# Kernel optimization log

Measured on AMD Instinct MI355X. Metric: run time of the kernel, lower is better.

Reference implementation:

```python
import jax, jax.numpy as jnp
import numpy as np

B, L, C = 16, 450, 768
MID = 256
K = 8912
TEMP = 0.07
ENT_TEMP = 0.01
EPS_NORM = 1e-12


def _l2norm(v):
    n = jnp.sqrt(jnp.sum(v * v, axis=-1, keepdims=True))
    return v / jnp.maximum(n, EPS_NORM)


def setup_inputs() -> dict:
    key = jax.random.key(0)
    k1, k2, k3, k4 = jax.random.split(key, 4)
    x = jax.random.normal(k1, (B, L, C), dtype=jnp.float32)
    W_down = jax.random.normal(k2, (C, MID), dtype=jnp.float32) * (1.0 / np.sqrt(C))
    b_down = jnp.zeros((MID,), dtype=jnp.float32)
    bound = 1.0 / np.sqrt(MID)
    embedding = jax.random.uniform(k3, (K, MID), dtype=jnp.float32, minval=-bound, maxval=bound)
    return {"x": x, "W_down": W_down, "b_down": b_down, "embedding": embedding}


def reference(x, W_down, b_down, embedding):
    Bx, Lx, Cx = x.shape
    # down projection: [B,L,C] -> [B,L,MID]
    z = jnp.einsum('blc,cm->blm', x, W_down) + b_down
    zf = z.reshape(Bx * Lx, MID)
    zn = _l2norm(zf)                       # [N, MID]
    en = _l2norm(embedding)                # [K, MID]
    # squared euclidean distance on the unit sphere: ||a-b||^2 = 2 - 2 a.b
    d = 2.0 - 2.0 * jnp.einsum('nm,km->nk', zn, en)   # [N, K]
    idx = jnp.argmin(d, axis=1)            # [N]
    # codebook usage (no-grad stats)
    occ = jnp.bincount(idx, length=K)
    code_book_usage = jnp.mean((occ > 0).astype(jnp.float32))
    # soft assignment probs (hard_quant branch)
    logits = -d / TEMP
    probs = jax.nn.softmax(logits, axis=1)
    z_q = en[idx]                          # [N, MID]
    vq_loss = jnp.mean((z_q - jax.lax.stop_gradient(zn)) ** 2)
    commit_loss = jnp.mean((jax.lax.stop_gradient(z_q) - zn) ** 2)
    # straight-through estimator
    z_q_ste = zn + jax.lax.stop_gradient(z_q - zn)
    # entropy loss on affinity = -d at entropy temperature
    fa = -d / ENT_TEMP
    p = jax.nn.softmax(fa, axis=-1)
    lp = jax.nn.log_softmax(fa, axis=-1)
    avg_probs = jnp.mean(p, axis=0)
    avg_entropy = -jnp.sum(avg_probs * jnp.log(avg_probs + 1e-5))
    sample_entropy = -jnp.mean(jnp.sum(p * lp, axis=-1))
    entropy_loss = sample_entropy - avg_entropy
    return (z_q_ste.reshape(Bx, Lx, MID), probs.reshape(Bx, Lx, K),
            code_book_usage, vq_loss, commit_loss, entropy_loss)
```

## Files before the change

### kernel.cpp

```cpp
#include <hip/hip_runtime.h>
#include <stdint.h>

#define N_TOK 7200
#define N_PAD 7232
#define K_CODE 8912
#define K_PAD 8960
#define N_KT 140
#define MID 256
#define C_DIM 768
#define INV_TEMP (1.0f/0.07f)
#define INV_ETEMP 100.0f
#define MARGIN 0.02f
#define CAND_CAP 64
#define EPS_N 1e-12f

typedef __attribute__((ext_vector_type(8))) short short8;
typedef __attribute__((ext_vector_type(4))) float f32x4;

__device__ __forceinline__ unsigned short f2bf(float f) {
    unsigned u = __float_as_uint(f);
    u += 0x7fffu + ((u >> 16) & 1u);
    return (unsigned short)(u >> 16);
}
__device__ __forceinline__ float bf2f(unsigned short h) {
    return __uint_as_float(((unsigned)h) << 16);
}

__global__ void k_init(float* ap_acc, int* used, float* acc4, int* ccnt) {
    int i = blockIdx.x * 256 + threadIdx.x;
    if (i < K_CODE) { ap_acc[i] = 0.f; used[i] = 0; }
    if (i < N_TOK) ccnt[i] = 0;
    if (i < 4) acc4[i] = 0.f;
}

__global__ void k_wsplit(const float* __restrict__ W,
                         unsigned short* __restrict__ wt_h,
                         unsigned short* __restrict__ wt_l) {
    int i = blockIdx.x * 256 + threadIdx.x;
    if (i >= C_DIM * MID) return;
    int c = i / MID, t = i % MID;
    float v = W[i];
    unsigned short h = f2bf(v);
    unsigned short l = f2bf(v - bf2f(h));
    wt_h[t * C_DIM + c] = h;
    wt_l[t * C_DIM + c] = l;
}

__global__ void k_ennorm(const float* __restrict__ emb,
                         float* __restrict__ en,
                         unsigned short* __restrict__ en_h) {
    int n = blockIdx.x, t = threadIdx.x;
    float v = emb[n * MID + t];
    __shared__ float sb[256];
    sb[t] = v * v; __syncthreads();
    for (int s = 128; s > 0; s >>= 1) { if (t < s) sb[t] += sb[t + s]; __syncthreads(); }
    float nn = sqrtf(sb[0]);
    float o = v / fmaxf(nn, EPS_N);
    en[n * MID + t] = o;
    en_h[n * MID + t] = f2bf(o);
}

__global__ __launch_bounds__(256) void k_zgemm(const float* __restrict__ x,
                                               const unsigned short* __restrict__ wt_h,
                                               const unsigned short* __restrict__ wt_l,
                                               float* __restrict__ zbuf) {
    __shared__ unsigned short ls[4 * 64 * 72];
    unsigned short* xh = ls;
    unsigned short* xl = ls + 64 * 72;
    unsigned short* wh = ls + 2 * 64 * 72;
    unsigned short* wl = ls + 3 * 64 * 72;
    int tid = threadIdx.x;
    int m0 = blockIdx.y * 64;
    int t0 = blockIdx.x * 64;
    int lane = tid & 63, wv = tid >> 6;
    int quad = lane >> 4, l15 = lane & 15;
    int mrow0 = (wv >> 1) * 32, ncol0 = (wv & 1) * 32;
    f32x4 acc[2][2] = {};

    for (int ch = 0; ch < 12; ch++) {
        int c0 = ch * 64;
        for (int it = 0; it < 4; it++) {
            int r = it * 16 + (tid >> 4);
            int cq = tid & 15;
            float4 v = make_float4(0.f, 0.f, 0.f, 0.f);
            int gr = m0 + r;
            if (gr < N_TOK) v = ((const float4*)x)[(size_t)gr * (C_DIM / 4) + (c0 >> 2) + cq];
            unsigned short h0 = f2bf(v.x), h1 = f2bf(v.y), h2 = f2bf(v.z), h3 = f2bf(v.w);
            ushort4 hh = make_ushort4(h0, h1, h2, h3);
            ushort4 ll = make_ushort4(f2bf(v.x - bf2f(h0)), f2bf(v.y - bf2f(h1)),
                                      f2bf(v.z - bf2f(h2)), f2bf(v.w - bf2f(h3)));
            *((ushort4*)&xh[r * 72 + cq * 4]) = hh;
            *((ushort4*)&xl[r * 72 + cq * 4]) = ll;
        }
        for (int it = 0; it < 2; it++) {
            int r = it * 32 + (tid >> 3);
            int cq = tid & 7;
            uint4 vh = ((const uint4*)wt_h)[(size_t)(t0 + r) * (C_DIM / 8) + (c0 >> 3) + cq];
            uint4 vl = ((const uint4*)wt_l)[(size_t)(t0 + r) * (C_DIM / 8) + (c0 >> 3) + cq];
            *((uint4*)&wh[r * 72 + cq * 8]) = vh;
            *((uint4*)&wl[r * 72 + cq * 8]) = vl;
        }
        __syncthreads();
        for (int ks = 0; ks < 2; ks++) {
            int co = ks * 32 + quad * 8;
            short8 ah0 = *((const short8*)&xh[(mrow0 + l15) * 72 + co]);
            short8 ah1 = *((const short8*)&xh[(mrow0 + 16 + l15) * 72 + co]);
            short8 al0 = *((const short8*)&xl[(mrow0 + l15) * 72 + co]);
            short8 al1 = *((const short8*)&xl[(mrow0 + 16 + l15) * 72 + co]);
            short8 bh0 = *((const short8*)&wh[(ncol0 + l15) * 72 + co]);
            short8 bh1 = *((const short8*)&wh[(ncol0 + 16 + l15) * 72 + co]);
            short8 bl0 = *((const short8*)&wl[(ncol0 + l15) * 72 + co]);
            short8 bl1 = *((const short8*)&wl[(ncol0 + 16 + l15) * 72 + co]);
            acc[0][0] = __builtin_amdgcn_mfma_f32_16x16x32_bf16(ah0, bh0, acc[0][0], 0, 0, 0);
            acc[0][1] = __builtin_amdgcn_mfma_f32_16x16x32_bf16(ah0, bh1, acc[0][1], 0, 0, 0);
            acc[1][0] = __builtin_amdgcn_mfma_f32_16x16x32_bf16(ah1, bh0, acc[1][0], 0, 0, 0);
            acc[1][1] = __builtin_amdgcn_mfma_f32_16x16x32_bf16(ah1, bh1, acc[1][1], 0, 0, 0);
            acc[0][0] = __builtin_amdgcn_mfma_f32_16x16x32_bf16(ah0, bl0, acc[0][0], 0, 0, 0);
            acc[0][1] = __builtin_amdgcn_mfma_f32_16x16x32_bf16(ah0, bl1, acc[0][1], 0, 0, 0);
            acc[1][0] = __builtin_amdgcn_mfma_f32_16x16x32_bf16(ah1, bl0, acc[1][0], 0, 0, 0);
            acc[1][1] = __builtin_amdgcn_mfma_f32_16x16x32_bf16(ah1, bl1, acc[1][1], 0, 0, 0);
            acc[0][0] = __builtin_amdgcn_mfma_f32_16x16x32_bf16(al0, bh0, acc[0][0], 0, 0, 0);
            acc[0][1] = __builtin_amdgcn_mfma_f32_16x16x32_bf16(al0, bh1, acc[0][1], 0, 0, 0);
            acc[1][0] = __builtin_amdgcn_mfma_f32_16x16x32_bf16(al1, bh0, acc[1][0], 0, 0, 0);
            acc[1][1] = __builtin_amdgcn_mfma_f32_16x16x32_bf16(al1, bh1, acc[1][1], 0, 0, 0);
        }
        __syncthreads();
    }
    for (int i = 0; i < 2; i++)
        for (int j = 0; j < 2; j++)
            for (int r = 0; r < 4; r++) {
                int gr = m0 + mrow0 + i * 16 + quad * 4 + r;
                int gc = t0 + ncol0 + j * 16 + l15;
                if (gr < N_TOK) zbuf[(size_t)gr * MID + gc] = acc[i][j][r];
            }
}

__global__ void k_znorm(float* __restrict__ zbuf, const float* __restrict__ b_down,
                        unsigned short* __restrict__ zn_h) {
    int n = blockIdx.x, t = threadIdx.x;
    float v = zbuf[(size_t)n * MID + t] + b_down[t];
    __shared__ float sb[256];
    sb[t] = v * v; __syncthreads();
    for (int s = 128; s > 0; s >>= 1) { if (t < s) sb[t] += sb[t + s]; __syncthreads(); }
    float nn = sqrtf(sb[0]);
    float o = v / fmaxf(nn, EPS_N);
    zbuf[(size_t)n * MID + t] = o;
    zn_h[(size_t)n * MID + t] = f2bf(o);
}

template<int PASS>
__global__ __launch_bounds__(256) void k_dpass(const unsigned short* __restrict__ zn_h,
                                               const unsigned short* __restrict__ en_h,
                                               float4* __restrict__ part4,
                                               const float* __restrict__ rs_m,
                                               const float* __restrict__ rs_ist,
                                               const float* __restrict__ rs_is1,
                                               float* __restrict__ ap_acc,
                                               float* __restrict__ out1,
                                               int* __restrict__ ccnt,
                                               int* __restrict__ cand) {
    __shared__ __align__(16) char smem[2 * 64 * 136 * 2];
    unsigned short* at = (unsigned short*)smem;
    unsigned short* bt = at + 64 * 136;
    int tid = threadIdx.x;
    int kt = blockIdx.x, mt = blockIdx.y;
    int m0 = mt * 64, k0c = kt * 64;
    int lane = tid & 63, wv = tid >> 6;
    int quad = lane >> 4, l15 = lane & 15;
    int mrow0 = (wv >> 1) * 32, ncol0 = (wv & 1) * 32;
    f32x4 acc[2][2] = {};

    for (int ch = 0; ch < 2; ch++) {
        int c0 = ch * 128;
        for (int it = 0; it < 4; it++) {
            int r = it * 16 + (tid >> 4);
            int cq = tid & 15;
            uint4 va = ((const uint4*)zn_h)[(size_t)(m0 + r) * (MID / 8) + (c0 >> 3) + cq];
            uint4 vb = ((const uint4*)en_h)[(size_t)(k0c + r) * (MID / 8) + (c0 >> 3) + cq];
            *((uint4*)&at[r * 136 + cq * 8]) = va;
            *((uint4*)&bt[r * 136 + cq * 8]) = vb;
        }
        __syncthreads();
        for (int ks = 0; ks < 4; ks++) {
            int co = ks * 32 + quad * 8;
            short8 a0 = *((const short8*)&at[(mrow0 + l15) * 136 + co]);
            short8 a1 = *((const short8*)&at[(mrow0 + 16 + l15) * 136 + co]);
            short8 b0 = *((const short8*)&bt[(ncol0 + l15) * 136 + co]);
            short8 b1 = *((const short8*)&bt[(ncol0 + 16 + l15) * 136 + co]);
            acc[0][0] = __builtin_amdgcn_mfma_f32_16x16x32_bf16(a0, b0, acc[0][0], 0, 0, 0);
            acc[0][1] = __builtin_amdgcn_mfma_f32_16x16x32_bf16(a0, b1, acc[0][1], 0, 0, 0);
            acc[1][0] = __builtin_amdgcn_mfma_f32_16x16x32_bf16(a1, b0, acc[1][0], 0, 0, 0);
            acc[1][1] = __builtin_amdgcn_mfma_f32_16x16x32_bf16(a1, b1, acc[1][1], 0, 0, 0);
        }
        __syncthreads();
    }

    float* sd = (float*)smem;
    float* lm = sd + 64 * 68;
    float* lt = lm + 64;
    float* l1 = lt + 64;
    float* colacc = l1 + 64;

    if (PASS == 2) {
        if (tid < 64) {
            int gr = m0 + tid;
            bool okr = gr < N_TOK;
            lm[tid] = okr ? rs_m[gr] : 0.f;
            lt[tid] = okr ? rs_ist[gr] : 0.f;
            l1[tid] = okr ? rs_is1[gr] : 0.f;
        }
    }
    for (int i = 0; i < 2; i++)
        for (int j = 0; j < 2; j++)
            for (int r = 0; r < 4; r++) {
                int lr = mrow0 + i * 16 + quad * 4 + r;
                int lc = ncol0 + j * 16 + l15;
                int gc = k0c + lc;
                float dv = (gc < K_CODE) ? (2.f - 2.f * acc[i][j][r]) : 1e30f;
                sd[lr * 68 + lc] = dv;
            }
    __syncthreads();

    if (PASS == 1) {
        int rloc = wv * 16 + (lane >> 2);
        const float* rowp = sd + rloc * 68 + (lane & 3) * 16;
        float vals[16];
        float vmin = 1e30f;
        #pragma unroll
        for (int i = 0; i < 16; i++) { vals[i] = rowp[i]; vmin = fminf(vmin, vals[i]); }
        vmin = fminf(vmin, __shfl_xor(vmin, 1));
        vmin = fminf(vmin, __shfl_xor(vmin, 2));
        float st = 0.f, s1 = 0.f, s2 = 0.f;
        #pragma unroll
        for (int i = 0; i < 16; i++) {
            float dd = vmin - vals[i];
            st += __expf(dd * INV_TEMP);
            float te = dd * INV_ETEMP;
            float e = __expf(te);
            s1 += e; s2 += e * te;
        }
        st += __shfl_xor(st, 1); st += __shfl_xor(st, 2);
        s1 += __shfl_xor(s1, 1); s1 += __shfl_xor(s1, 2);
        s2 += __shfl_xor(s2, 1); s2 += __shfl_xor(s2, 2);
        if ((lane & 3) == 0) {
            int gr = m0 + rloc;
            if (gr < N_TOK) part4[(size_t)gr * N_KT + kt] = make_float4(vmin, st, s1, s2);
        }
    } else {
        int col = tid & 63, rq = tid >> 6;
        float ce = 0.f;
        #pragma unroll
        for (int r16 = 0; r16 < 16; r16++) {
            int lr = rq * 16 + r16;
            float dv = sd[lr * 68 + col];
            ce += __expf((lm[lr] - dv) * INV_ETEMP) * l1[lr];
        }
        colacc[rq * 64 + col] = ce;
        __syncthreads();
        if (tid < 64) {
            float s = colacc[tid] + colacc[64 + tid] + colacc[128 + tid] + colacc[192 + tid];
            int gc = k0c + tid;
            if (gc < K_CODE) atomicAdd(&ap_acc[gc], s);
        }
        #pragma unroll
        for (int it = 0; it < 4; it++) {
            int idx = it * 256 + tid;
            int lr = idx >> 4, c4 = idx & 15;
            int gr = m0 + lr;
            if (gr >= N_TOK) continue;
            int gc = k0c + c4 * 4;
            if (gc >= K_CODE) continue;
            float4 v = *((const float4*)(sd + lr * 68 + c4 * 4));
            float mm = lm[lr], tt = lt[lr];
            float thr = mm + MARGIN;
            if (v.x <= thr) { int p = atomicAdd(&ccnt[gr], 1); if (p < CAND_CAP) cand[gr * CAND_CAP + p] = gc + 0; }
            if (v.y <= thr) { int p = atomicAdd(&ccnt[gr], 1); if (p < CAND_CAP) cand[gr * CAND_CAP + p] = gc + 1; }
            if (v.z <= thr) { int p = atomicAdd(&ccnt[gr], 1); if (p < CAND_CAP) cand[gr * CAND_CAP + p] = gc + 2; }
            if (v.w <= thr) { int p = atomicAdd(&ccnt[gr], 1); if (p < CAND_CAP) cand[gr * CAND_CAP + p] = gc + 3; }
            float4 p;
            p.x = __expf((mm - v.x) * INV_TEMP) * tt;
            p.y = __expf((mm - v.y) * INV_TEMP) * tt;
            p.z = __expf((mm - v.z) * INV_TEMP) * tt;
            p.w = __expf((mm - v.w) * INV_TEMP) * tt;
            *((float4*)(out1 + (size_t)gr * K_CODE + gc)) = p;
        }
    }
}

__global__ void k_combine(const float4* __restrict__ part4,
                          float* __restrict__ rs_m, float* __restrict__ rs_ist,
                          float* __restrict__ rs_is1,
                          float* __restrict__ acc4) {
    int sub = threadIdx.x >> 6;
    int row = blockIdx.x * 4 + sub;
    int l = threadIdx.x & 63;
    float4 pv[3];
    float m = 1e30f;
    #pragma unroll
    for (int c = 0; c < 3; c++) {
        int t = l + c * 64;
        pv[c] = (t < N_KT) ? part4[(size_t)row * N_KT + t] : make_float4(1e30f, 0.f, 0.f, 0.f);
        m = fminf(m, pv[c].x);
    }
    #pragma unroll
    for (int s = 1; s < 64; s <<= 1) m = fminf(m, __shfl_xor(m, s));
    float st = 0.f, s1 = 0.f, s2 = 0.f;
    #pragma unroll
    for (int c = 0; c < 3; c++) {
        float mb = pv[c].x;
        int t = l + c * 64;
        if (t < N_KT && mb < 1e29f) {
            float dT = (m - mb) * INV_TEMP;
            st += __expf(dT) * pv[c].y;
            float dE = (m - mb) * INV_ETEMP;
            float e = __expf(dE);
            s1 += e * pv[c].z;
            s2 += e * (pv[c].w + dE * pv[c].z);
        }
    }
    #pragma unroll
    for (int s = 1; s < 64; s <<= 1) {
        st += __shfl_xor(st, s);
        s1 += __shfl_xor(s1, s);
        s2 += __shfl_xor(s2, s);
    }
    if (l == 0) {
        rs_m[row] = m;
        rs_ist[row] = 1.f / st;
        rs_is1[row] = 1.f / s1;
        atomicAdd(&acc4[1], s2 / s1 - __logf(s1));
    }
}

__global__ void k_refine(const float* __restrict__ zn, const float* __restrict__ en,
                         const int* __restrict__ ccnt, const int* __restrict__ cand,
                         int* __restrict__ idxb, int* __restrict__ used,
                         float* __restrict__ acc4) {
    int n = blockIdx.x * 4 + (threadIdx.x >> 6);
    int lane = threadIdx.x & 63;
    if (n >= N_TOK) return;
    int cnt = ccnt[n];
    if (cnt > CAND_CAP) cnt = CAND_CAP;
    float4 a = ((const float4*)(zn + (size_t)n * MID))[lane];
    float best = 1e30f; int bj = K_CODE;
    for (int c = 0; c < cnt; c++) {
        int code = cand[n * CAND_CAP + c];
        float4 b = ((const float4*)(en + (size_t)code * MID))[lane];
        float s = a.x * b.x + a.y * b.y + a.z * b.z + a.w * b.w;
        #pragma unroll
        for (int off = 1; off < 64; off <<= 1) s += __shfl_xor(s, off);
        float dist = 2.f - 2.f * s;
        if (dist < best || (dist == best && code < bj)) { best = dist; bj = code; }
    }
    float4 b = ((const float4*)(en + (size_t)bj * MID))[lane];
    float dx = b.x - a.x, dy = b.y - a.y, dz = b.z - a.z, dw = b.w - a.w;
    float sq = dx * dx + dy * dy + dz * dz + dw * dw;
    #pragma unroll
    for (int off = 32; off > 0; off >>= 1) sq += __shfl_down(sq, off);
    if (lane == 0) {
        idxb[n] = bj;
        used[bj] = 1;
        atomicAdd(&acc4[0], sq);
    }
}

__global__ void k_out0(const float* __restrict__ en, const int* __restrict__ idxb,
                       float* __restrict__ out0) {
    int n = blockIdx.x, t = threadIdx.x;
    int j = idxb[n];
    out0[(size_t)n * MID + t] = en[(size_t)j * MID + t];
}

__global__ void k_scal(const int* __restrict__ used, const float* __restrict__ ap_acc,
                       const float* __restrict__ acc4, float* __restrict__ outs) {
    int t = threadIdx.x;
    float uSum = 0.f, aeSum = 0.f;
    for (int k = t; k < K_CODE; k += 256) {
        uSum += (float)used[k];
        float ap = ap_acc[k] * (1.0f / (float)N_TOK);
        aeSum += ap * __logf(ap + 1e-5f);
    }
    __shared__ float sb[256];
    sb[t] = uSum; __syncthreads();
    for (int s = 128; s > 0; s >>= 1) { if (t < s) sb[t] += sb[t + s]; __syncthreads(); }
    uSum = sb[0];
    __syncthreads(); sb[t] = aeSum; __syncthreads();
    for (int s = 128; s > 0; s >>= 1) { if (t < s) sb[t] += sb[t + s]; __syncthreads(); }
    aeSum = sb[0];
    if (t == 0) {
        outs[0] = uSum / (float)K_CODE;
        float vq = acc4[0] / (float)((size_t)N_TOK * MID);
        outs[1] = vq;
        outs[2] = vq;
        outs[3] = -(acc4[1] / (float)N_TOK) + aeSum;
    }
}

extern "C" void kernel_launch(void* const* d_in, const int* in_sizes, int n_in,
                              void* d_out, int out_size, void* d_ws, size_t ws_size,
                              hipStream_t stream) {
    const float* x   = (const float*)d_in[0];
    const float* W   = (const float*)d_in[1];
    const float* b   = (const float*)d_in[2];
    const float* emb = (const float*)d_in[3];

    float* out  = (float*)d_out;
    float* out0 = out;
    float* out1 = out + (size_t)N_TOK * MID;
    float* outs = out + (size_t)N_TOK * MID + (size_t)N_TOK * K_CODE;

    char* w = (char*)d_ws;
    size_t off = 0;
    auto carve = [&](size_t bytes) { void* p = w + off; off += (bytes + 255) & ~(size_t)255; return p; };
    float*          zn    = (float*)         carve((size_t)N_PAD * MID * 4);
    float*          en    = (float*)         carve((size_t)K_PAD * MID * 4);
    unsigned short* zn_h  = (unsigned short*)carve((size_t)N_PAD * MID * 2);
    unsigned short* en_h  = (unsigned short*)carve((size_t)K_PAD * MID * 2);
    unsigned short* wt_h  = (unsigned short*)carve((size_t)MID * C_DIM * 2);
    unsigned short* wt_l  = (unsigned short*)carve((size_t)MID * C_DIM * 2);
    float4*         part4 = (float4*)        carve((size_t)N_TOK * N_KT * 16);
    float*          rs_m  = (float*)         carve((size_t)N_TOK * 4);
    float*          rs_ist= (float*)         carve((size_t)N_TOK * 4);
    float*          rs_is1= (float*)         carve((size_t)N_TOK * 4);
    int*            ccnt  = (int*)           carve((size_t)N_TOK * 4);
    int*            cand  = (int*)           carve((size_t)N_TOK * CAND_CAP * 4);
    int*            idxb  = (int*)           carve((size_t)N_TOK * 4);
    float*          ap_acc= (float*)         carve((size_t)K_CODE * 4);
    int*            used  = (int*)           carve((size_t)K_CODE * 4);
    float*          acc4  = (float*)         carve(16);
    (void)ws_size; (void)in_sizes; (void)n_in; (void)out_size;

    k_init   <<<35, 256, 0, stream>>>(ap_acc, used, acc4, ccnt);
    k_wsplit <<<(C_DIM * MID + 255) / 256, 256, 0, stream>>>(W, wt_h, wt_l);
    k_ennorm <<<K_CODE, 256, 0, stream>>>(emb, en, en_h);
    k_zgemm  <<<dim3(4, 113), 256, 0, stream>>>(x, wt_h, wt_l, zn);
    k_znorm  <<<N_TOK, 256, 0, stream>>>(zn, b, zn_h);
    k_dpass<1><<<dim3(N_KT, 113), 256, 0, stream>>>(zn_h, en_h, part4, rs_m, rs_ist, rs_is1, ap_acc, out1, ccnt, cand);
    k_combine<<<N_TOK / 4, 256, 0, stream>>>(part4, rs_m, rs_ist, rs_is1, acc4);
    k_dpass<2><<<dim3(N_KT, 113), 256, 0, stream>>>(zn_h, en_h, part4, rs_m, rs_ist, rs_is1, ap_acc, out1, ccnt, cand);
    k_refine <<<N_TOK / 4, 256, 0, stream>>>(zn, en, ccnt, cand, idxb, used, acc4);
    k_out0   <<<N_TOK, 256, 0, stream>>>(en, idxb, out0);
    k_scal   <<<1, 256, 0, stream>>>(used, ap_acc, acc4, outs);
}
```

Before: 671.1 us.

## Enlarge distance GEMM tiles to 128x128 and fuse epilogues in registers

The two distance passes now use 128x128 block tiles, with each wave owning a 64x64 sub-tile of 4x4 MFMA accumulators. The epilogues work straight from registers instead of first staging the distance tile in shared memory. Pass 1 folds per-wave partial softmax stats into a per-row partial for each k-tile, which halves the part4 traffic and the combine work. Pass 2 writes probabilities directly as scalar stores and reduces column sums with shuffles. The codebook gather for out0 is merged into the refine kernel, removing one launch. The costs are higher register pressure, uncoalesced scalar output stores and fewer blocks.

```diff
diff --git a/kernel.cpp b/kernel.cpp
--- a/kernel.cpp
+++ b/kernel.cpp
@@ -2,10 +2,11 @@
 #include <stdint.h>
 
 #define N_TOK 7200
-#define N_PAD 7232
+#define N_PAD 7296
 #define K_CODE 8912
 #define K_PAD 8960
-#define N_KT 140
+#define N_KT 70
+#define N_MT 57
 #define MID 256
 #define C_DIM 768
 #define INV_TEMP (1.0f/0.07f)
@@ -13,6 +14,7 @@
 #define MARGIN 0.02f
 #define CAND_CAP 64
 #define EPS_N 1e-12f
+#define LDT 136
 
 typedef __attribute__((ext_vector_type(8))) short short8;
 typedef __attribute__((ext_vector_type(4))) float f32x4;
@@ -159,130 +161,143 @@
                                                float* __restrict__ out1,
                                                int* __restrict__ ccnt,
                                                int* __restrict__ cand) {
-    __shared__ __align__(16) char smem[2 * 64 * 136 * 2];
-    unsigned short* at = (unsigned short*)smem;
-    unsigned short* bt = at + 64 * 136;
+    __shared__ __align__(16) unsigned short ab_s[2 * 128 * LDT];
+    __shared__ float rs_s[3 * 128];
+    unsigned short* a_s = ab_s;
+    unsigned short* b_s = ab_s + 128 * LDT;
     int tid = threadIdx.x;
     int kt = blockIdx.x, mt = blockIdx.y;
-    int m0 = mt * 64, k0c = kt * 64;
-    int lane = tid & 63, wv = tid >> 6;
+    int m0 = mt * 128, k0 = kt * 128;
+    int lane = tid & 63, w = tid >> 6;
     int quad = lane >> 4, l15 = lane & 15;
-    int mrow0 = (wv >> 1) * 32, ncol0 = (wv & 1) * 32;
-    f32x4 acc[2][2] = {};
+    int wrow = (w >> 1) * 64, wcol = (w & 1) * 64;
+    f32x4 acc[4][4] = {};
+
+    if (PASS == 2 && tid < 128) {
+        int gr = m0 + tid;
+        bool ok = gr < N_TOK;
+        rs_s[tid]       = ok ? rs_m[gr]   : 0.f;
+        rs_s[128 + tid] = ok ? rs_ist[gr] : 0.f;
+        rs_s[256 + tid] = ok ? rs_is1[gr] : 0.f;
+    }
 
     for (int ch = 0; ch < 2; ch++) {
-        int c0 = ch * 128;
-        for (int it = 0; it < 4; it++) {
-            int r = it * 16 + (tid >> 4);
-            int cq = tid & 15;
-            uint4 va = ((const uint4*)zn_h)[(size_t)(m0 + r) * (MID / 8) + (c0 >> 3) + cq];
-            uint4 vb = ((const uint4*)en_h)[(size_t)(k0c + r) * (MID / 8) + (c0 >> 3) + cq];
-            *((uint4*)&at[r * 136 + cq * 8]) = va;
-            *((uint4*)&bt[r * 136 + cq * 8]) = vb;
+        #pragma unroll
+        for (int it = 0; it < 8; it++) {
+            int lin = it * 256 + tid;
+            int r = lin >> 4, c16 = lin & 15;
+            uint4 va = ((const uint4*)zn_h)[(size_t)(m0 + r) * 32 + ch * 16 + c16];
+            uint4 vb = ((const uint4*)en_h)[(size_t)(k0 + r) * 32 + ch * 16 + c16];
+            *((uint4*)&a_s[r * LDT + c16 * 8]) = va;
+            *((uint4*)&b_s[r * LDT + c16 * 8]) = vb;
         }
         __syncthreads();
+        #pragma unroll
         for (int ks = 0; ks < 4; ks++) {
             int co = ks * 32 + quad * 8;
-            short8 a0 = *((const short8*)&at[(mrow0 + l15) * 136 + co]);
-            short8 a1 = *((const short8*)&at[(mrow0 + 16 + l15) * 136 + co]);
-            short8 b0 = *((const short8*)&bt[(ncol0 + l15) * 136 + co]);
-            short8 b1 = *((const short8*)&bt[(ncol0 + 16 + l15) * 136 + co]);
-            acc[0][0] = __builtin_amdgcn_mfma_f32_16x16x32_bf16(a0, b0, acc[0][0], 0, 0, 0);
-            acc[0][1] = __builtin_amdgcn_mfma_f32_16x16x32_bf16(a0, b1, acc[0][1], 0, 0, 0);
-            acc[1][0] = __builtin_amdgcn_mfma_f32_16x16x32_bf16(a1, b0, acc[1][0], 0, 0, 0);
-            acc[1][1] = __builtin_amdgcn_mfma_f32_16x16x32_bf16(a1, b1, acc[1][1], 0, 0, 0);
+            short8 af[4], bfr[4];
+            #pragma unroll
+            for (int i = 0; i < 4; i++) af[i]  = *((const short8*)&a_s[(wrow + i * 16 + l15) * LDT + co]);
+            #pragma unroll
+            for (int j = 0; j < 4; j++) bfr[j] = *((const short8*)&b_s[(wcol + j * 16 + l15) * LDT + co]);
+            #pragma unroll
+            for (int i = 0; i < 4; i++)
+                #pragma unroll
+                for (int j = 0; j < 4; j++)
+                    acc[i][j] = __builtin_amdgcn_mfma_f32_16x16x32_bf16(af[i], bfr[j], acc[i][j], 0, 0, 0);
         }
         __syncthreads();
     }
 
-    float* sd = (float*)smem;
-    float* lm = sd + 64 * 68;
-    float* lt = lm + 64;
-    float* l1 = lt + 64;
-    float* colacc = l1 + 64;
-
-    if (PASS == 2) {
-        if (tid < 64) {
+    bool okc[4];
+    #pragma unroll
+    for (int j = 0; j < 4; j++) okc[j] = (k0 + wcol + j * 16 + l15) < K_CODE;
+    #pragma unroll
+    for (int i = 0; i < 4; i++)
+        #pragma unroll
+        for (int j = 0; j < 4; j++)
+            #pragma unroll
+            for (int r = 0; r < 4; r++)
+                acc[i][j][r] = okc[j] ? (2.f - 2.f * acc[i][j][r]) : 1e30f;
+
+    if (PASS == 1) {
+        float4* p_s = (float4*)ab_s;
+        #pragma unroll
+        for (int i = 0; i < 4; i++)
+            #pragma unroll
+            for (int r = 0; r < 4; r++) {
+                int lr = wrow + i * 16 + quad * 4 + r;
+                float v0 = acc[i][0][r], v1 = acc[i][1][r], v2 = acc[i][2][r], v3 = acc[i][3][r];
+                float vmin = fminf(fminf(v0, v1), fminf(v2, v3));
+                float st = 0.f, s1 = 0.f, s2 = 0.f;
+                #pragma unroll
+                for (int j = 0; j < 4; j++) {
+                    float dd = vmin - acc[i][j][r];
+                    st += __expf(dd * INV_TEMP);
+                    float te = dd * INV_ETEMP;
+                    float e = __expf(te);
+                    s1 += e; s2 += e * te;
+                }
+                p_s[lr * 33 + (w & 1) * 16 + l15] = make_float4(vmin, st, s1, s2);
+            }
+        __syncthreads();
+        if (tid < 128) {
+            const float4* rowp = (const float4*)ab_s + tid * 33;
+            float m = 1e30f;
+            #pragma unroll
+            for (int p = 0; p < 32; p++) m = fminf(m, rowp[p].x);
+            float st = 0.f, s1 = 0.f, s2 = 0.f;
+            #pragma unroll
+            for (int p = 0; p < 32; p++) {
+                float4 v = rowp[p];
+                if (v.x < 1e29f) {
+                    float dT = (m - v.x) * INV_TEMP;
+                    st += __expf(dT) * v.y;
+                    float dE = (m - v.x) * INV_ETEMP;
+                    float e = __expf(dE);
+                    s1 += e * v.z;
+                    s2 += e * (v.w + dE * v.z);
+                }
+            }
             int gr = m0 + tid;
-            bool okr = gr < N_TOK;
-            lm[tid] = okr ? rs_m[gr] : 0.f;
-            lt[tid] = okr ? rs_ist[gr] : 0.f;
-            l1[tid] = okr ? rs_is1[gr] : 0.f;
-        }
-    }
-    for (int i = 0; i < 2; i++)
-        for (int j = 0; j < 2; j++)
+            if (gr < N_TOK) part4[(size_t)gr * N_KT + kt] = make_float4(m, st, s1, s2);
+        }
+    } else {
+        float colsum[4] = {0.f, 0.f, 0.f, 0.f};
+        #pragma unroll
+        for (int i = 0; i < 4; i++)
+            #pragma unroll
             for (int r = 0; r < 4; r++) {
-                int lr = mrow0 + i * 16 + quad * 4 + r;
-                int lc = ncol0 + j * 16 + l15;
-                int gc = k0c + lc;
-                float dv = (gc < K_CODE) ? (2.f - 2.f * acc[i][j][r]) : 1e30f;
-                sd[lr * 68 + lc] = dv;
+                int lr = wrow + i * 16 + quad * 4 + r;
+                int gr = m0 + lr;
+                if (gr >= N_TOK) continue;
+                float mm = rs_s[lr], tt = rs_s[128 + lr], o1 = rs_s[256 + lr];
+                float thr = mm + MARGIN;
+                float* orow = out1 + (size_t)gr * K_CODE;
+                #pragma unroll
+                for (int j = 0; j < 4; j++) {
+                    if (!okc[j]) continue;
+                    int gc = k0 + wcol + j * 16 + l15;
+                    float dv = acc[i][j][r];
+                    if (dv <= thr) {
+                        int p = atomicAdd(&ccnt[gr], 1);
+                        if (p < CAND_CAP) cand[gr * CAND_CAP + p] = gc;
+                    }
+                    orow[gc] = __expf((mm - dv) * INV_TEMP) * tt;
+                    colsum[j] += __expf((mm - dv) * INV_ETEMP) * o1;
+                }
             }
-    __syncthreads();
-
-    if (PASS == 1) {
-        int rloc = wv * 16 + (lane >> 2);
-        const float* rowp = sd + rloc * 68 + (lane & 3) * 16;
-        float vals[16];
-        float vmin = 1e30f;
-        #pragma unroll
-        for (int i = 0; i < 16; i++) { vals[i] = rowp[i]; vmin = fminf(vmin, vals[i]); }
-        vmin = fminf(vmin, __shfl_xor(vmin, 1));
-        vmin = fminf(vmin, __shfl_xor(vmin, 2));
-        float st = 0.f, s1 = 0.f, s2 = 0.f;
-        #pragma unroll
-        for (int i = 0; i < 16; i++) {
-            float dd = vmin - vals[i];
-            st += __expf(dd * INV_TEMP);
-            float te = dd * INV_ETEMP;
-            float e = __expf(te);
-            s1 += e; s2 += e * te;
-        }
-        st += __shfl_xor(st, 1); st += __shfl_xor(st, 2);
-        s1 += __shfl_xor(s1, 1); s1 += __shfl_xor(s1, 2);
-        s2 += __shfl_xor(s2, 1); s2 += __shfl_xor(s2, 2);
-        if ((lane & 3) == 0) {
-            int gr = m0 + rloc;
-            if (gr < N_TOK) part4[(size_t)gr * N_KT + kt] = make_float4(vmin, st, s1, s2);
-        }
-    } else {
-        int col = tid & 63, rq = tid >> 6;
-        float ce = 0.f;
-        #pragma unroll
-        for (int r16 = 0; r16 < 16; r16++) {
-            int lr = rq * 16 + r16;
-            float dv = sd[lr * 68 + col];
-            ce += __expf((lm[lr] - dv) * INV_ETEMP) * l1[lr];
-        }
-        colacc[rq * 64 + col] = ce;
-        __syncthreads();
-        if (tid < 64) {
-            float s = colacc[tid] + colacc[64 + tid] + colacc[128 + tid] + colacc[192 + tid];
-            int gc = k0c + tid;
-            if (gc < K_CODE) atomicAdd(&ap_acc[gc], s);
-        }
-        #pragma unroll
-        for (int it = 0; it < 4; it++) {
-            int idx = it * 256 + tid;
-            int lr = idx >> 4, c4 = idx & 15;
-            int gr = m0 + lr;
-            if (gr >= N_TOK) continue;
-            int gc = k0c + c4 * 4;
-            if (gc >= K_CODE) continue;
-            float4 v = *((const float4*)(sd + lr * 68 + c4 * 4));
-            float mm = lm[lr], tt = lt[lr];
-            float thr = mm + MARGIN;
-            if (v.x <= thr) { int p = atomicAdd(&ccnt[gr], 1); if (p < CAND_CAP) cand[gr * CAND_CAP + p] = gc + 0; }
-            if (v.y <= thr) { int p = atomicAdd(&ccnt[gr], 1); if (p < CAND_CAP) cand[gr * CAND_CAP + p] = gc + 1; }
-            if (v.z <= thr) { int p = atomicAdd(&ccnt[gr], 1); if (p < CAND_CAP) cand[gr * CAND_CAP + p] = gc + 2; }
-            if (v.w <= thr) { int p = atomicAdd(&ccnt[gr], 1); if (p < CAND_CAP) cand[gr * CAND_CAP + p] = gc + 3; }
-            float4 p;
-            p.x = __expf((mm - v.x) * INV_TEMP) * tt;
-            p.y = __expf((mm - v.y) * INV_TEMP) * tt;
-            p.z = __expf((mm - v.z) * INV_TEMP) * tt;
-            p.w = __expf((mm - v.w) * INV_TEMP) * tt;
-            *((float4*)(out1 + (size_t)gr * K_CODE + gc)) = p;
+        #pragma unroll
+        for (int j = 0; j < 4; j++) {
+            colsum[j] += __shfl_xor(colsum[j], 16);
+            colsum[j] += __shfl_xor(colsum[j], 32);
+        }
+        if (quad == 0) {
+            #pragma unroll
+            for (int j = 0; j < 4; j++) {
+                int gc = k0 + wcol + j * 16 + l15;
+                if (gc < K_CODE) atomicAdd(&ap_acc[gc], colsum[j]);
+            }
         }
     }
 }
@@ -294,10 +309,10 @@
     int sub = threadIdx.x >> 6;
     int row = blockIdx.x * 4 + sub;
     int l = threadIdx.x & 63;
-    float4 pv[3];
+    float4 pv[2];
     float m = 1e30f;
     #pragma unroll
-    for (int c = 0; c < 3; c++) {
+    for (int c = 0; c < 2; c++) {
         int t = l + c * 64;
         pv[c] = (t < N_KT) ? part4[(size_t)row * N_KT + t] : make_float4(1e30f, 0.f, 0.f, 0.f);
         m = fminf(m, pv[c].x);
@@ -306,7 +321,7 @@
     for (int s = 1; s < 64; s <<= 1) m = fminf(m, __shfl_xor(m, s));
     float st = 0.f, s1 = 0.f, s2 = 0.f;
     #pragma unroll
-    for (int c = 0; c < 3; c++) {
+    for (int c = 0; c < 2; c++) {
         float mb = pv[c].x;
         int t = l + c * 64;
         if (t < N_KT && mb < 1e29f) {
@@ -335,7 +350,7 @@
 __global__ void k_refine(const float* __restrict__ zn, const float* __restrict__ en,
                          const int* __restrict__ ccnt, const int* __restrict__ cand,
                          int* __restrict__ idxb, int* __restrict__ used,
-                         float* __restrict__ acc4) {
+                         float* __restrict__ acc4, float* __restrict__ out0) {
     int n = blockIdx.x * 4 + (threadIdx.x >> 6);
     int lane = threadIdx.x & 63;
     if (n >= N_TOK) return;
@@ -353,6 +368,7 @@
         if (dist < best || (dist == best && code < bj)) { best = dist; bj = code; }
     }
     float4 b = ((const float4*)(en + (size_t)bj * MID))[lane];
+    ((float4*)(out0 + (size_t)n * MID))[lane] = b;
     float dx = b.x - a.x, dy = b.y - a.y, dz = b.z - a.z, dw = b.w - a.w;
     float sq = dx * dx + dy * dy + dz * dz + dw * dw;
     #pragma unroll
@@ -362,13 +378,6 @@
         used[bj] = 1;
         atomicAdd(&acc4[0], sq);
     }
-}
-
-__global__ void k_out0(const float* __restrict__ en, const int* __restrict__ idxb,
-                       float* __restrict__ out0) {
-    int n = blockIdx.x, t = threadIdx.x;
-    int j = idxb[n];
-    out0[(size_t)n * MID + t] = en[(size_t)j * MID + t];
 }
 
 __global__ void k_scal(const int* __restrict__ used, const float* __restrict__ ap_acc,
@@ -435,10 +444,9 @@
     k_ennorm <<<K_CODE, 256, 0, stream>>>(emb, en, en_h);
     k_zgemm  <<<dim3(4, 113), 256, 0, stream>>>(x, wt_h, wt_l, zn);
     k_znorm  <<<N_TOK, 256, 0, stream>>>(zn, b, zn_h);
-    k_dpass<1><<<dim3(N_KT, 113), 256, 0, stream>>>(zn_h, en_h, part4, rs_m, rs_ist, rs_is1, ap_acc, out1, ccnt, cand);
+    k_dpass<1><<<dim3(N_KT, N_MT), 256, 0, stream>>>(zn_h, en_h, part4, rs_m, rs_ist, rs_is1, ap_acc, out1, ccnt, cand);
     k_combine<<<N_TOK / 4, 256, 0, stream>>>(part4, rs_m, rs_ist, rs_is1, acc4);
-    k_dpass<2><<<dim3(N_KT, 113), 256, 0, stream>>>(zn_h, en_h, part4, rs_m, rs_ist, rs_is1, ap_acc, out1, ccnt, cand);
-    k_refine <<<N_TOK / 4, 256, 0, stream>>>(zn, en, ccnt, cand, idxb, used, acc4);
-    k_out0   <<<N_TOK, 256, 0, stream>>>(en, idxb, out0);
+    k_dpass<2><<<dim3(N_KT, N_MT), 256, 0, stream>>>(zn_h, en_h, part4, rs_m, rs_ist, rs_is1, ap_acc, out1, ccnt, cand);
+    k_refine <<<N_TOK / 4, 256, 0, stream>>>(zn, en, ccnt, cand, idxb, used, acc4, out0);
     k_scal   <<<1, 256, 0, stream>>>(used, ap_acc, acc4, outs);
 }
```

New measurement: 692.3 us. 1.03x slower.
